# Kernel tuning notes

Hardware: AMD Instinct MI355X
Metric: run time of the kernel (lower is better)

Reference implementation:

```python
import jax, jax.numpy as jnp
import numpy as np

EPS = 1e-5
H = 128
NA = 300000
NB = 600000
NBRS = 6

def _bn(x, gamma, beta):
    # BatchNorm1d in training mode: batch stats over dim 0, biased variance
    mu = jnp.mean(x, axis=0)
    var = jnp.mean((x - mu) ** 2, axis=0)
    return gamma * (x - mu) * jax.lax.rsqrt(var + EPS) + beta

def _lin(x, w, b):
    return x @ w.T + b

def setup_inputs() -> dict:
    key = jax.random.key(0)
    ks = jax.random.split(key, 20)
    s = 1.0 / np.sqrt(H)
    d = {
        'atom_layer_input': jax.random.normal(ks[0], (NA, H), jnp.float32),
        'bond_layer_input': jax.random.normal(ks[1], (NB, H), jnp.float32),
        'atom_adjacency_graph': jax.random.randint(ks[2], (NA, NBRS), 0, NA, jnp.int32),
        'atom_bond_adjacency_graph': jax.random.randint(ks[3], (NA, NBRS), 0, NB, jnp.int32),
        'bond_atom_adjacency_graph': jax.random.randint(ks[4], (NB, 2), 0, NA, jnp.int32),
    }
    names = ['U', 'V', 'A', 'B', 'C']
    for i, n in enumerate(names):
        d[n + '_w'] = jax.random.uniform(ks[5 + 2 * i], (H, H), jnp.float32, -s, s)
        d[n + '_b'] = jax.random.uniform(ks[6 + 2 * i], (H,), jnp.float32, -s, s)
    d['bn_bond_gamma'] = jnp.ones((H,), jnp.float32)
    d['bn_bond_beta'] = jnp.zeros((H,), jnp.float32)
    d['bn_atom_gamma'] = jnp.ones((H,), jnp.float32)
    d['bn_atom_beta'] = jnp.zeros((H,), jnp.float32)
    return d

def reference(atom_layer_input, bond_layer_input, atom_adjacency_graph,
              atom_bond_adjacency_graph, bond_atom_adjacency_graph,
              U_w, U_b, V_w, V_b, A_w, A_b, B_w, B_b, C_w, C_b,
              bn_bond_gamma, bn_bond_beta, bn_atom_gamma, bn_atom_beta):
    # --- edge (bond) update ---
    ex = atom_layer_input[bond_atom_adjacency_graph[:, 0]]  # [NB, H]
    ey = atom_layer_input[bond_atom_adjacency_graph[:, 1]]  # [NB, H]
    edge_syn = _lin(bond_layer_input, A_w, A_b) + _lin(ex, B_w, B_b) + _lin(ey, C_w, C_b)
    edge_gates = jax.nn.sigmoid(edge_syn)                    # [NB, H]
    edge_syn_bn = _bn(edge_syn, bn_bond_gamma, bn_bond_beta)
    bond_layer_output = jax.nn.relu(edge_syn_bn)             # residual overwritten in source
    # --- node (atom) update ---
    nbr_feats = atom_layer_input[atom_adjacency_graph]       # [NA, 6, H] gather
    nbr_V = jnp.einsum('nkh,oh->nko', nbr_feats, V_w) + V_b  # [NA, 6, H]
    nbr_gates = edge_gates[atom_bond_adjacency_graph]        # [NA, 6, H] gather
    msg = jnp.sum(nbr_gates * nbr_V, axis=1)                 # [NA, H]
    atom_syn = _lin(atom_layer_input, U_w, U_b) + msg
    atom_syn_bn = _bn(atom_syn, bn_atom_gamma, bn_atom_beta)
    atom_layer_output = jax.nn.relu(atom_syn_bn) + atom_layer_input  # residual (atom_feature_dim==0)
    return (atom_layer_output, bond_layer_output)
```

## Files before the change

### kernel.cpp

```cpp
#include <hip/hip_runtime.h>
#include <hip/hip_bf16.h>


#define H   128
#define NA  300000
#define NB  600000
#define EPS 1e-5f

#define NTILE_A (NA / 32)
#define NTILE_B (NB / 32)
#define GRID_A  512
#define GRID_B  1024
#define EGRID   2048
#define LDSW    136

typedef __attribute__((ext_vector_type(4)))  float  f32x4;
typedef __attribute__((ext_vector_type(16))) float  f32x16;
typedef __attribute__((ext_vector_type(8)))  __bf16 bfv8;
typedef __attribute__((ext_vector_type(8)))  unsigned short u16x8;

static __device__ __forceinline__ unsigned short f2bf(float f) {
    unsigned u = __float_as_uint(f);
    u = (u + 0x7fffu + ((u >> 16) & 1u)) >> 16;
    return (unsigned short)u;
}
static __device__ __forceinline__ float bf2f(unsigned short s) {
    return __uint_as_float(((unsigned)s) << 16);
}

static __device__ __forceinline__ u16x8 pack2(f32x4 a, f32x4 b) {
    u16x8 w;
#pragma unroll
    for (int i = 0; i < 4; i++) { w[i] = f2bf(a[i]); w[i + 4] = f2bf(b[i]); }
    return w;
}

static __device__ __forceinline__ bfv8 load_frag(const float* __restrict__ p) {
    f32x4 a = *(const f32x4*)p, b = *(const f32x4*)(p + 4);
    bfv8 f;
#pragma unroll
    for (int i = 0; i < 4; i++) { f[i] = (__bf16)a[i]; f[i + 4] = (__bf16)b[i]; }
    return f;
}

__global__ __launch_bounds__(512, 4) void k_atom_gemm(
    const float* __restrict__ X,
    const float* __restrict__ Uw, const float* __restrict__ Vw,
    const float* __restrict__ Bw, const float* __restrict__ Cw,
    unsigned short* __restrict__ Uxo, unsigned short* __restrict__ Vxo,
    unsigned short* __restrict__ Bxo, unsigned short* __restrict__ Cxo)
{
    __shared__ unsigned short xs[2][32 * LDSW];
    __shared__ unsigned short es[2][32 * LDSW];

    const int tid   = threadIdx.x;
    const int lane  = tid & 63;
    const int w     = tid >> 6;
    const int ng    = w & 3;
    const int pair  = w >> 2;
    const int l31   = lane & 31;
    const int khalf = lane >> 5;

    const int wrow_off = (ng * 32 + l31) * H + khalf * 8;
    const int cperm    = ng * 32 + khalf * 16;

    const float* W0 = pair ? Bw : Uw;
    const float* W1 = pair ? Cw : Vw;

    bfv8 aw0[8], aw1[8];
#pragma unroll
    for (int k = 0; k < 8; k++) {
        aw0[k] = load_frag(W0 + wrow_off + k * 16);
        aw1[k] = load_frag(W1 + wrow_off + k * 16);
    }

    const int srow = tid >> 4, sseg = tid & 15;
    const int g = tid >> 8, ft = tid & 255;
    const int frow = ft >> 3, fseg = ft & 7;
    unsigned short* O0 = g ? Bxo : Uxo;
    unsigned short* O1 = g ? Cxo : Vxo;

    const int stride = gridDim.x;
    int t = blockIdx.x;

    f32x4 sl0, sl1;
    {
        const float* sp = X + (size_t)(t * 32 + srow) * H + sseg * 8;
        sl0 = *(const f32x4*)sp; sl1 = *(const f32x4*)(sp + 4);
    }
    *(u16x8*)&xs[0][srow * LDSW + sseg * 8] = pack2(sl0, sl1);
    __syncthreads();

    int p = 0;
#pragma unroll 1
    for (; t < NTILE_A; ) {
        const int tn = t + stride;
        const bool have = tn < NTILE_A;
        if (have) {
            const float* sp = X + (size_t)(tn * 32 + srow) * H + sseg * 8;
            sl0 = *(const f32x4*)sp; sl1 = *(const f32x4*)(sp + 4);
        }

        const unsigned short* xrow = &xs[p][l31 * LDSW + khalf * 8];
        unsigned short*       esw  = &es[pair][l31 * LDSW + cperm];
        const unsigned short* esr  = &es[g][frow * LDSW + fseg * 16];
        const size_t fbase = (size_t)(t * 32 + frow) * H + fseg * 16;

        {
            f32x16 acc;
#pragma unroll
            for (int i = 0; i < 16; i++) acc[i] = 0.0f;
#pragma unroll
            for (int k = 0; k < 8; k++) {
                bfv8 xf = *(const bfv8*)(xrow + k * 16);
                acc = __builtin_amdgcn_mfma_f32_32x32x16_bf16(aw0[k], xf, acc, 0, 0, 0);
            }
            u16x8 o0, o1;
#pragma unroll
            for (int v = 0; v < 8; v++) { o0[v] = f2bf(acc[v]); o1[v] = f2bf(acc[v + 8]); }
            *(u16x8*)esw       = o0;
            *(u16x8*)(esw + 8) = o1;
        }
        __syncthreads();

        f32x16 acc1;
#pragma unroll
        for (int i = 0; i < 16; i++) acc1[i] = 0.0f;
#pragma unroll
        for (int k = 0; k < 8; k++) {
            bfv8 xf = *(const bfv8*)(xrow + k * 16);
            acc1 = __builtin_amdgcn_mfma_f32_32x32x16_bf16(aw1[k], xf, acc1, 0, 0, 0);
        }
        {
            u16x8 e0 = *(const u16x8*)esr, e1 = *(const u16x8*)(esr + 8);
            *(u16x8*)(O0 + fbase)     = e0;
            *(u16x8*)(O0 + fbase + 8) = e1;
        }
        __syncthreads();

        {
            u16x8 o0, o1;
#pragma unroll
            for (int v = 0; v < 8; v++) { o0[v] = f2bf(acc1[v]); o1[v] = f2bf(acc1[v + 8]); }
            *(u16x8*)esw       = o0;
            *(u16x8*)(esw + 8) = o1;
        }
        __syncthreads();

        {
            u16x8 e0 = *(const u16x8*)esr, e1 = *(const u16x8*)(esr + 8);
            *(u16x8*)(O1 + fbase)     = e0;
            *(u16x8*)(O1 + fbase + 8) = e1;
        }
        if (have)
            *(u16x8*)&xs[p ^ 1][srow * LDSW + sseg * 8] = pack2(sl0, sl1);
        __syncthreads();
        p ^= 1;
        t = tn;
    }
}

__global__ __launch_bounds__(256, 4) void k_bond_gemm(
    const float* __restrict__ Xb,
    const float* __restrict__ Aw, const float* __restrict__ Ab,
    const float* __restrict__ Bb, const float* __restrict__ Cb,
    const int* __restrict__ g2,
    const unsigned short* __restrict__ Bx, const unsigned short* __restrict__ Cx,
    unsigned short* __restrict__ esyn,
    float* __restrict__ psum, float* __restrict__ psq)
{
    __shared__ unsigned short xs[2][32 * LDSW];
    __shared__ unsigned short es[32 * LDSW];
    __shared__ float bias_s[128];

    const int tid   = threadIdx.x;
    const int lane  = tid & 63;
    const int ng    = tid >> 6;
    const int l31   = lane & 31;
    const int khalf = lane >> 5;
    const int cperm = ng * 32 + khalf * 16;

    bfv8 aw[8];
    const float* wr = Aw + (ng * 32 + l31) * H + khalf * 8;
#pragma unroll
    for (int k = 0; k < 8; k++) aw[k] = load_frag(wr + k * 16);

    if (tid < 128) {
        const int pcol = tid;
        const int grp = pcol >> 5, r = pcol & 31, kh = r >> 4, wi = r & 15;
        const int ct = grp * 32 + (wi >> 2) * 8 + kh * 4 + (wi & 3);
        bias_s[pcol] = Ab[ct] + Bb[ct] + Cb[ct];
    }

    const int srow = tid >> 3, sseg = tid & 7;

    float fs[16], fq[16];
#pragma unroll
    for (int i = 0; i < 16; i++) { fs[i] = 0.f; fq[i] = 0.f; }

    const int stride = gridDim.x;
    int t = blockIdx.x;

    f32x4 sl[4];
    {
        const float* sp = Xb + (size_t)(t * 32 + srow) * H + sseg * 16;
#pragma unroll
        for (int i = 0; i < 4; i++) sl[i] = *(const f32x4*)(sp + 4 * i);
    }
    {
        unsigned short* d = &xs[0][srow * LDSW + sseg * 16];
        *(u16x8*)d       = pack2(sl[0], sl[1]);
        *(u16x8*)(d + 8) = pack2(sl[2], sl[3]);
    }
    int2 ggf = *(const int2*)(g2 + 2 * (size_t)(t * 32 + srow));
    __syncthreads();

    int p = 0;
#pragma unroll 1
    for (; t < NTILE_B; ) {
        const int tn = t + stride;
        const bool have = tn < NTILE_B;

        if (have) {
            const float* sp = Xb + (size_t)(tn * 32 + srow) * H + sseg * 16;
#pragma unroll
            for (int i = 0; i < 4; i++) sl[i] = *(const f32x4*)(sp + 4 * i);
        }

        {
            const unsigned short* xrow = &xs[p][l31 * LDSW + khalf * 8];
            f32x16 acc;
#pragma unroll
            for (int i = 0; i < 16; i++) acc[i] = 0.0f;
#pragma unroll
            for (int k = 0; k < 8; k++) {
                bfv8 xf = *(const bfv8*)(xrow + k * 16);
                acc = __builtin_amdgcn_mfma_f32_32x32x16_bf16(aw[k], xf, acc, 0, 0, 0);
            }
            u16x8 o0, o1;
#pragma unroll
            for (int v = 0; v < 8; v++) { o0[v] = f2bf(acc[v]); o1[v] = f2bf(acc[v + 8]); }
            unsigned short* esw = &es[l31 * LDSW + cperm];
            *(u16x8*)esw       = o0;
            *(u16x8*)(esw + 8) = o1;
        }

        const unsigned short* bxp = Bx + (size_t)ggf.x * H + sseg * 16;
        const unsigned short* cxp = Cx + (size_t)ggf.y * H + sseg * 16;
        u16x8 b0 = *(const u16x8*)bxp, b1 = *(const u16x8*)(bxp + 8);
        u16x8 c0 = *(const u16x8*)cxp, c1 = *(const u16x8*)(cxp + 8);
        if (have) ggf = *(const int2*)(g2 + 2 * (size_t)(tn * 32 + srow));
        __syncthreads();

        {
            const unsigned short* esr = &es[srow * LDSW + sseg * 16];
            u16x8 e0 = *(const u16x8*)esr, e1 = *(const u16x8*)(esr + 8);
            const float* bp = bias_s + sseg * 16;
            u16x8 w0, w1;
#pragma unroll
            for (int i = 0; i < 8; i++) {
                float v = bf2f(e0[i]) + bp[i] + bf2f(b0[i]) + bf2f(c0[i]);
                w0[i] = f2bf(v); fs[i] += v; fq[i] += v * v;
            }
#pragma unroll
            for (int i = 0; i < 8; i++) {
                float v = bf2f(e1[i]) + bp[8 + i] + bf2f(b1[i]) + bf2f(c1[i]);
                w1[i] = f2bf(v); fs[8 + i] += v; fq[8 + i] += v * v;
            }
            unsigned short* op = esyn + (size_t)(t * 32 + srow) * H + sseg * 16;
            *(u16x8*)op       = w0;
            *(u16x8*)(op + 8) = w1;
        }

        if (have) {
            unsigned short* d = &xs[p ^ 1][srow * LDSW + sseg * 16];
            *(u16x8*)d       = pack2(sl[0], sl[1]);
            *(u16x8*)(d + 8) = pack2(sl[2], sl[3]);
        }
        __syncthreads();
        p ^= 1;
        t = tn;
    }

    float* red = (float*)es;
    for (int i = 0; i < 16; i++) {
        __syncthreads();
        red[tid] = fs[i]; red[256 + tid] = fq[i];
        __syncthreads();
        if (tid < 8) {
            float S = 0.f, Q = 0.f;
            for (int r = 0; r < 32; r++) { S += red[r * 8 + tid]; Q += red[256 + r * 8 + tid]; }
            psum[(size_t)blockIdx.x * H + tid * 16 + i] = S;
            psq [(size_t)blockIdx.x * H + tid * 16 + i] = Q;
        }
    }
}

__global__ void k_bn_stats(const float* __restrict__ psum, const float* __restrict__ psq,
                           int nblk, float invN,
                           const float* __restrict__ gamma, const float* __restrict__ beta,
                           float* __restrict__ scale, float* __restrict__ shift)
{
    __shared__ float ls[256], lq[256];
    const int c = blockIdx.x;
    float s = 0.f, q = 0.f;
    for (int i = threadIdx.x; i < nblk; i += 256) {
        s += psum[(size_t)i * H + c];
        q += psq [(size_t)i * H + c];
    }
    ls[threadIdx.x] = s; lq[threadIdx.x] = q;
    __syncthreads();
    for (int off = 128; off > 0; off >>= 1) {
        if ((int)threadIdx.x < off) {
            ls[threadIdx.x] += ls[threadIdx.x + off];
            lq[threadIdx.x] += lq[threadIdx.x + off];
        }
        __syncthreads();
    }
    if (threadIdx.x == 0) {
        const int r = c & 31, kh = r >> 4, wi = r & 15;
        const int ct = (c & ~31) + (wi >> 2) * 8 + kh * 4 + (wi & 3);
        float mean = ls[0] * invN;
        float var  = lq[0] * invN - mean * mean;
        float sc   = gamma[ct] * rsqrtf(var + EPS);
        scale[c] = sc;
        shift[c] = beta[ct] - mean * sc;
    }
}

__global__ __launch_bounds__(256) void k_bond_out(const unsigned short* __restrict__ esyn,
                                                  float* __restrict__ y,
                                                  const float* __restrict__ scale,
                                                  const float* __restrict__ shift)
{
    const size_t total  = (size_t)NB * (H / 8);
    const size_t stride = (size_t)gridDim.x * 256;
    const int c0 = (threadIdx.x & 15) * 8;
    const f32x4 sc0 = *(const f32x4*)(scale + c0), sc1 = *(const f32x4*)(scale + c0 + 4);
    const f32x4 sh0 = *(const f32x4*)(shift + c0), sh1 = *(const f32x4*)(shift + c0 + 4);
    const int tc0 = (c0 & ~31) + (((c0 >> 2) & 3) * 8) + ((c0 >> 4) & 1) * 4;
    const int tc1 = tc0 + 8;
    for (size_t i = (size_t)blockIdx.x * 256 + threadIdx.x; i < total; i += stride) {
        u16x8 v = ((const u16x8*)esyn)[i];
        const size_t row = i >> 4;
        f32x4 o0, o1;
#pragma unroll
        for (int j = 0; j < 4; j++) {
            o0[j] = fmaxf(bf2f(v[j])     * sc0[j] + sh0[j], 0.0f);
            o1[j] = fmaxf(bf2f(v[j + 4]) * sc1[j] + sh1[j], 0.0f);
        }
        float* yp = y + row * H;
        *(f32x4*)(yp + tc0) = o0;
        *(f32x4*)(yp + tc1) = o1;
    }
}

__global__ __launch_bounds__(256) void k_atom_msg(
    const unsigned short* __restrict__ Ux,
    const unsigned short* __restrict__ Vx,
    const unsigned short* __restrict__ esyn,
    const int* __restrict__ adj,
    const int* __restrict__ abadj,
    const float* __restrict__ Ub, const float* __restrict__ Vb,
    unsigned short* __restrict__ syn_a,
    float* __restrict__ psum, float* __restrict__ psq)
{
    const int cg = threadIdx.x & 15;
    const int rh = threadIdx.x >> 4;
    const int c0 = cg * 8;
    const int tc0 = (c0 & ~31) + (((c0 >> 2) & 3) * 8) + ((c0 >> 4) & 1) * 4;
    const f32x4 ub0 = *(const f32x4*)(Ub + tc0), ub1 = *(const f32x4*)(Ub + tc0 + 8);
    const f32x4 vb0 = *(const f32x4*)(Vb + tc0), vb1 = *(const f32x4*)(Vb + tc0 + 8);

    float s[8], q[8];
#pragma unroll
    for (int j = 0; j < 8; j++) { s[j] = 0.f; q[j] = 0.f; }

    const int rstride = gridDim.x * 16;
    int r = blockIdx.x * 16 + rh;

    int2 A[3], Bv[3];
    if (r < NA) {
#pragma unroll
        for (int p = 0; p < 3; p++) {
            A[p]  = *(const int2*)(adj   + (size_t)r * 6 + 2 * p);
            Bv[p] = *(const int2*)(abadj + (size_t)r * 6 + 2 * p);
        }
    }

#pragma unroll 1
    for (; r < NA; ) {
        const int rn = r + rstride;

        const int ai[6] = {A[0].x, A[0].y, A[1].x, A[1].y, A[2].x, A[2].y};
        const int bi[6] = {Bv[0].x, Bv[0].y, Bv[1].x, Bv[1].y, Bv[2].x, Bv[2].y};

        u16x8 uv = *(const u16x8*)(Ux + (size_t)r * H + c0);

        if (rn < NA) {
#pragma unroll
            for (int p = 0; p < 3; p++) {
                A[p]  = *(const int2*)(adj   + (size_t)rn * 6 + 2 * p);
                Bv[p] = *(const int2*)(abadj + (size_t)rn * 6 + 2 * p);
            }
        }

        float v[8];
#pragma unroll
        for (int j = 0; j < 4; j++) {
            v[j]     = bf2f(uv[j])     + ub0[j];
            v[j + 4] = bf2f(uv[j + 4]) + ub1[j];
        }
#pragma unroll
        for (int k = 0; k < 6; k++) {
            u16x8 vx = *(const u16x8*)(Vx   + (size_t)ai[k] * H + c0);
            u16x8 es = *(const u16x8*)(esyn + (size_t)bi[k] * H + c0);
#pragma unroll
            for (int j = 0; j < 4; j++) {
                float g0 = 1.0f / (1.0f + __expf(-bf2f(es[j])));
                float g1 = 1.0f / (1.0f + __expf(-bf2f(es[j + 4])));
                v[j]     += g0 * (bf2f(vx[j])     + vb0[j]);
                v[j + 4] += g1 * (bf2f(vx[j + 4]) + vb1[j]);
            }
        }
        u16x8 ov;
#pragma unroll
        for (int j = 0; j < 8; j++) ov[j] = f2bf(v[j]);
        *(u16x8*)(syn_a + (size_t)r * H + c0) = ov;
#pragma unroll
        for (int j = 0; j < 8; j++) { s[j] += v[j]; q[j] += v[j] * v[j]; }

        r = rn;
    }

    __shared__ float ls[256][8], lq[256][8];
#pragma unroll
    for (int j = 0; j < 8; j++) { ls[threadIdx.x][j] = s[j]; lq[threadIdx.x][j] = q[j]; }
    __syncthreads();
    if (threadIdx.x < 128) {
        const int c = threadIdx.x, g = c >> 3, j = c & 7;
        float S = 0.f, Q = 0.f;
        for (int rg = 0; rg < 16; rg++) { S += ls[rg * 16 + g][j]; Q += lq[rg * 16 + g][j]; }
        psum[(size_t)blockIdx.x * H + c] = S;
        psq [(size_t)blockIdx.x * H + c] = Q;
    }
}

__global__ __launch_bounds__(256) void k_atom_out(const unsigned short* __restrict__ syn,
                                                  const float* __restrict__ xin,
                                                  float* __restrict__ y,
                                                  const float* __restrict__ scale,
                                                  const float* __restrict__ shift)
{
    const size_t total  = (size_t)NA * (H / 8);
    const size_t stride = (size_t)gridDim.x * 256;
    const int c0 = (threadIdx.x & 15) * 8;
    const f32x4 sc0 = *(const f32x4*)(scale + c0), sc1 = *(const f32x4*)(scale + c0 + 4);
    const f32x4 sh0 = *(const f32x4*)(shift + c0), sh1 = *(const f32x4*)(shift + c0 + 4);
    const int tc0 = (c0 & ~31) + (((c0 >> 2) & 3) * 8) + ((c0 >> 4) & 1) * 4;
    const int tc1 = tc0 + 8;
    for (size_t i = (size_t)blockIdx.x * 256 + threadIdx.x; i < total; i += stride) {
        u16x8 v = ((const u16x8*)syn)[i];
        const size_t row = i >> 4;
        const float* xp = xin + row * H;
        f32x4 x0 = *(const f32x4*)(xp + tc0), x1 = *(const f32x4*)(xp + tc1);
        f32x4 o0, o1;
#pragma unroll
        for (int j = 0; j < 4; j++) {
            o0[j] = fmaxf(bf2f(v[j])     * sc0[j] + sh0[j], 0.0f) + x0[j];
            o1[j] = fmaxf(bf2f(v[j + 4]) * sc1[j] + sh1[j], 0.0f) + x1[j];
        }
        float* yp = y + row * H;
        *(f32x4*)(yp + tc0) = o0;
        *(f32x4*)(yp + tc1) = o1;
    }
}

extern "C" void kernel_launch(void* const* d_in, const int* in_sizes, int n_in,
                              void* d_out, int out_size, void* d_ws, size_t ws_size,
                              hipStream_t stream)
{
    const float* X     = (const float*)d_in[0];
    const float* Xb    = (const float*)d_in[1];
    const int*   adj   = (const int*)d_in[2];
    const int*   abadj = (const int*)d_in[3];
    const int*   g2    = (const int*)d_in[4];
    const float* Uw = (const float*)d_in[5],  *Ub = (const float*)d_in[6];
    const float* Vw = (const float*)d_in[7],  *Vb = (const float*)d_in[8];
    const float* Aw = (const float*)d_in[9],  *Ab = (const float*)d_in[10];
    const float* Bw = (const float*)d_in[11], *Bb = (const float*)d_in[12];
    const float* Cw = (const float*)d_in[13], *Cb = (const float*)d_in[14];
    const float* gb = (const float*)d_in[15], *bb = (const float*)d_in[16];
    const float* ga = (const float*)d_in[17], *ba = (const float*)d_in[18];

    float* out_atom = (float*)d_out;
    float* out_bond = out_atom + (size_t)NA * H;

    char* ws = (char*)d_ws;
    size_t o = 0;
    unsigned short* Ux    = (unsigned short*)(ws + o); o += (size_t)NA * H * 2;
    unsigned short* Vx    = (unsigned short*)(ws + o); o += (size_t)NA * H * 2;
    unsigned short* Bx    = (unsigned short*)(ws + o); o += (size_t)NA * H * 2;
    unsigned short* Cx    = (unsigned short*)(ws + o); o += (size_t)NA * H * 2;
    unsigned short* esyn  = (unsigned short*)(ws + o); o += (size_t)NB * H * 2;
    unsigned short* syn_a = (unsigned short*)(ws + o); o += (size_t)NA * H * 2;
    float* psum_b = (float*)(ws + o);  o += (size_t)EGRID * H * 4;
    float* psq_b  = (float*)(ws + o);  o += (size_t)EGRID * H * 4;
    float* psum_a = (float*)(ws + o);  o += (size_t)EGRID * H * 4;
    float* psq_a  = (float*)(ws + o);  o += (size_t)EGRID * H * 4;
    float* scale_b = (float*)(ws + o); o += 512;
    float* shift_b = (float*)(ws + o); o += 512;
    float* scale_a = (float*)(ws + o); o += 512;
    float* shift_a = (float*)(ws + o); o += 512;
    (void)o; (void)ws_size; (void)in_sizes; (void)n_in; (void)out_size;

    k_atom_gemm<<<GRID_A, 512, 0, stream>>>(X, Uw, Vw, Bw, Cw, Ux, Vx, Bx, Cx);
    k_bond_gemm<<<GRID_B, 256, 0, stream>>>(Xb, Aw, Ab, Bb, Cb, g2, Bx, Cx, esyn,
                                            psum_b, psq_b);
    k_bn_stats<<<H, 256, 0, stream>>>(psum_b, psq_b, GRID_B, 1.0f / NB, gb, bb, scale_b, shift_b);
    k_bond_out<<<EGRID, 256, 0, stream>>>(esyn, out_bond, scale_b, shift_b);
    k_atom_msg<<<EGRID, 256, 0, stream>>>(Ux, Vx, esyn, adj, abadj, Ub, Vb, syn_a, psum_a, psq_a);
    k_bn_stats<<<H, 256, 0, stream>>>(psum_a, psq_a, EGRID, 1.0f / NA, ga, ba, scale_a, shift_a);
    k_atom_out<<<EGRID, 256, 0, stream>>>(syn_a, X, out_atom, scale_a, shift_a);
}
```

Before: 604.3 us.

## Fuse bond output and atom message kernels into one grid; add nontemporal streaming

```diff
diff --git a/kernel.cpp b/kernel.cpp
--- a/kernel.cpp
+++ b/kernel.cpp
@@ -9,9 +9,12 @@
 
 #define NTILE_A (NA / 32)
 #define NTILE_B (NB / 32)
-#define GRID_A  512
-#define GRID_B  1024
+#define GRID_A  1024
+#define GRID_B  1536
 #define EGRID   2048
+#define BOUT_BLKS 768
+#define MSG_BLKS  1280
+#define FUSED_GRID (BOUT_BLKS + MSG_BLKS)
 #define LDSW    136
 
 typedef __attribute__((ext_vector_type(4)))  float  f32x4;
@@ -26,6 +29,13 @@
 }
 static __device__ __forceinline__ float bf2f(unsigned short s) {
     return __uint_as_float(((unsigned)s) << 16);
+}
+
+static __device__ __forceinline__ f32x4 nt_load4(const float* p) {
+    return __builtin_nontemporal_load((const f32x4*)p);
+}
+static __device__ __forceinline__ void nt_store4(float* p, f32x4 v) {
+    __builtin_nontemporal_store(v, (f32x4*)p);
 }
 
 static __device__ __forceinline__ u16x8 pack2(f32x4 a, f32x4 b) {
@@ -86,7 +96,7 @@
     f32x4 sl0, sl1;
     {
         const float* sp = X + (size_t)(t * 32 + srow) * H + sseg * 8;
-        sl0 = *(const f32x4*)sp; sl1 = *(const f32x4*)(sp + 4);
+        sl0 = nt_load4(sp); sl1 = nt_load4(sp + 4);
     }
     *(u16x8*)&xs[0][srow * LDSW + sseg * 8] = pack2(sl0, sl1);
     __syncthreads();
@@ -98,7 +108,7 @@
         const bool have = tn < NTILE_A;
         if (have) {
             const float* sp = X + (size_t)(tn * 32 + srow) * H + sseg * 8;
-            sl0 = *(const f32x4*)sp; sl1 = *(const f32x4*)(sp + 4);
+            sl0 = nt_load4(sp); sl1 = nt_load4(sp + 4);
         }
 
         const unsigned short* xrow = &xs[p][l31 * LDSW + khalf * 8];
@@ -205,7 +215,7 @@
     {
         const float* sp = Xb + (size_t)(t * 32 + srow) * H + sseg * 16;
 #pragma unroll
-        for (int i = 0; i < 4; i++) sl[i] = *(const f32x4*)(sp + 4 * i);
+        for (int i = 0; i < 4; i++) sl[i] = nt_load4(sp + 4 * i);
     }
     {
         unsigned short* d = &xs[0][srow * LDSW + sseg * 16];
@@ -224,7 +234,7 @@
         if (have) {
             const float* sp = Xb + (size_t)(tn * 32 + srow) * H + sseg * 16;
 #pragma unroll
-            for (int i = 0; i < 4; i++) sl[i] = *(const f32x4*)(sp + 4 * i);
+            for (int i = 0; i < 4; i++) sl[i] = nt_load4(sp + 4 * i);
         }
 
         {
@@ -328,43 +338,45 @@
     }
 }
 
-__global__ __launch_bounds__(256) void k_bond_out(const unsigned short* __restrict__ esyn,
-                                                  float* __restrict__ y,
-                                                  const float* __restrict__ scale,
-                                                  const float* __restrict__ shift)
-{
-    const size_t total  = (size_t)NB * (H / 8);
-    const size_t stride = (size_t)gridDim.x * 256;
-    const int c0 = (threadIdx.x & 15) * 8;
-    const f32x4 sc0 = *(const f32x4*)(scale + c0), sc1 = *(const f32x4*)(scale + c0 + 4);
-    const f32x4 sh0 = *(const f32x4*)(shift + c0), sh1 = *(const f32x4*)(shift + c0 + 4);
-    const int tc0 = (c0 & ~31) + (((c0 >> 2) & 3) * 8) + ((c0 >> 4) & 1) * 4;
-    const int tc1 = tc0 + 8;
-    for (size_t i = (size_t)blockIdx.x * 256 + threadIdx.x; i < total; i += stride) {
-        u16x8 v = ((const u16x8*)esyn)[i];
-        const size_t row = i >> 4;
-        f32x4 o0, o1;
-#pragma unroll
-        for (int j = 0; j < 4; j++) {
-            o0[j] = fmaxf(bf2f(v[j])     * sc0[j] + sh0[j], 0.0f);
-            o1[j] = fmaxf(bf2f(v[j + 4]) * sc1[j] + sh1[j], 0.0f);
-        }
-        float* yp = y + row * H;
-        *(f32x4*)(yp + tc0) = o0;
-        *(f32x4*)(yp + tc1) = o1;
-    }
-}
-
-__global__ __launch_bounds__(256) void k_atom_msg(
+__global__ __launch_bounds__(256) void k_bout_amsg(
+    const unsigned short* __restrict__ esyn,
+    float* __restrict__ out_bond,
+    const float* __restrict__ scale, const float* __restrict__ shift,
     const unsigned short* __restrict__ Ux,
     const unsigned short* __restrict__ Vx,
-    const unsigned short* __restrict__ esyn,
     const int* __restrict__ adj,
     const int* __restrict__ abadj,
     const float* __restrict__ Ub, const float* __restrict__ Vb,
     unsigned short* __restrict__ syn_a,
     float* __restrict__ psum, float* __restrict__ psq)
 {
+    __shared__ float ls[256][8], lq[256][8];
+
+    if (blockIdx.x < BOUT_BLKS) {
+        const size_t total  = (size_t)NB * (H / 8);
+        const size_t stride = (size_t)BOUT_BLKS * 256;
+        const int c0 = (threadIdx.x & 15) * 8;
+        const f32x4 sc0 = *(const f32x4*)(scale + c0), sc1 = *(const f32x4*)(scale + c0 + 4);
+        const f32x4 sh0 = *(const f32x4*)(shift + c0), sh1 = *(const f32x4*)(shift + c0 + 4);
+        const int tc0 = (c0 & ~31) + (((c0 >> 2) & 3) * 8) + ((c0 >> 4) & 1) * 4;
+        const int tc1 = tc0 + 8;
+        for (size_t i = (size_t)blockIdx.x * 256 + threadIdx.x; i < total; i += stride) {
+            u16x8 v = ((const u16x8*)esyn)[i];
+            const size_t row = i >> 4;
+            f32x4 o0, o1;
+#pragma unroll
+            for (int j = 0; j < 4; j++) {
+                o0[j] = fmaxf(bf2f(v[j])     * sc0[j] + sh0[j], 0.0f);
+                o1[j] = fmaxf(bf2f(v[j + 4]) * sc1[j] + sh1[j], 0.0f);
+            }
+            float* yp = out_bond + row * H;
+            nt_store4(yp + tc0, o0);
+            nt_store4(yp + tc1, o1);
+        }
+        return;
+    }
+
+    const int bid = blockIdx.x - BOUT_BLKS;
     const int cg = threadIdx.x & 15;
     const int rh = threadIdx.x >> 4;
     const int c0 = cg * 8;
@@ -376,8 +388,8 @@
 #pragma unroll
     for (int j = 0; j < 8; j++) { s[j] = 0.f; q[j] = 0.f; }
 
-    const int rstride = gridDim.x * 16;
-    int r = blockIdx.x * 16 + rh;
+    const int rstride = MSG_BLKS * 16;
+    int r = bid * 16 + rh;
 
     int2 A[3], Bv[3];
     if (r < NA) {
@@ -433,7 +445,6 @@
         r = rn;
     }
 
-    __shared__ float ls[256][8], lq[256][8];
 #pragma unroll
     for (int j = 0; j < 8; j++) { ls[threadIdx.x][j] = s[j]; lq[threadIdx.x][j] = q[j]; }
     __syncthreads();
@@ -441,8 +452,8 @@
         const int c = threadIdx.x, g = c >> 3, j = c & 7;
         float S = 0.f, Q = 0.f;
         for (int rg = 0; rg < 16; rg++) { S += ls[rg * 16 + g][j]; Q += lq[rg * 16 + g][j]; }
-        psum[(size_t)blockIdx.x * H + c] = S;
-        psq [(size_t)blockIdx.x * H + c] = Q;
+        psum[(size_t)bid * H + c] = S;
+        psq [(size_t)bid * H + c] = Q;
     }
 }
 
@@ -463,7 +474,7 @@
         u16x8 v = ((const u16x8*)syn)[i];
         const size_t row = i >> 4;
         const float* xp = xin + row * H;
-        f32x4 x0 = *(const f32x4*)(xp + tc0), x1 = *(const f32x4*)(xp + tc1);
+        f32x4 x0 = nt_load4(xp + tc0), x1 = nt_load4(xp + tc1);
         f32x4 o0, o1;
 #pragma unroll
         for (int j = 0; j < 4; j++) {
@@ -471,8 +482,8 @@
             o1[j] = fmaxf(bf2f(v[j + 4]) * sc1[j] + sh1[j], 0.0f) + x1[j];
         }
         float* yp = y + row * H;
-        *(f32x4*)(yp + tc0) = o0;
-        *(f32x4*)(yp + tc1) = o1;
+        nt_store4(yp + tc0, o0);
+        nt_store4(yp + tc1, o1);
     }
 }
 
@@ -518,8 +529,9 @@
     k_bond_gemm<<<GRID_B, 256, 0, stream>>>(Xb, Aw, Ab, Bb, Cb, g2, Bx, Cx, esyn,
                                             psum_b, psq_b);
     k_bn_stats<<<H, 256, 0, stream>>>(psum_b, psq_b, GRID_B, 1.0f / NB, gb, bb, scale_b, shift_b);
-    k_bond_out<<<EGRID, 256, 0, stream>>>(esyn, out_bond, scale_b, shift_b);
-    k_atom_msg<<<EGRID, 256, 0, stream>>>(Ux, Vx, esyn, adj, abadj, Ub, Vb, syn_a, psum_a, psq_a);
-    k_bn_stats<<<H, 256, 0, stream>>>(psum_a, psq_a, EGRID, 1.0f / NA, ga, ba, scale_a, shift_a);
+    k_bout_amsg<<<FUSED_GRID, 256, 0, stream>>>(esyn, out_bond, scale_b, shift_b,
+                                                Ux, Vx, adj, abadj, Ub, Vb,
+                                                syn_a, psum_a, psq_a);
+    k_bn_stats<<<H, 256, 0, stream>>>(psum_a, psq_a, MSG_BLKS, 1.0f / NA, ga, ba, scale_a, shift_a);
     k_atom_out<<<EGRID, 256, 0, stream>>>(syn_a, X, out_atom, scale_a, shift_a);
 }
```

After: 669.9 us. 1.11x slower.

## Compute bond B/C projections in bond GEMM from gathered atom rows instead of precomputing

Applied to the files above, without the earlier changes.

```diff
diff --git a/kernel.cpp b/kernel.cpp
--- a/kernel.cpp
+++ b/kernel.cpp
@@ -46,9 +46,7 @@
 __global__ __launch_bounds__(512, 4) void k_atom_gemm(
     const float* __restrict__ X,
     const float* __restrict__ Uw, const float* __restrict__ Vw,
-    const float* __restrict__ Bw, const float* __restrict__ Cw,
-    unsigned short* __restrict__ Uxo, unsigned short* __restrict__ Vxo,
-    unsigned short* __restrict__ Bxo, unsigned short* __restrict__ Cxo)
+    unsigned short* __restrict__ Uxo, unsigned short* __restrict__ Vxo)
 {
     __shared__ unsigned short xs[2][32 * LDSW];
     __shared__ unsigned short es[2][32 * LDSW];
@@ -64,21 +62,15 @@
     const int wrow_off = (ng * 32 + l31) * H + khalf * 8;
     const int cperm    = ng * 32 + khalf * 16;
 
-    const float* W0 = pair ? Bw : Uw;
-    const float* W1 = pair ? Cw : Vw;
-
-    bfv8 aw0[8], aw1[8];
-#pragma unroll
-    for (int k = 0; k < 8; k++) {
-        aw0[k] = load_frag(W0 + wrow_off + k * 16);
-        aw1[k] = load_frag(W1 + wrow_off + k * 16);
-    }
+    const float* W = pair ? Vw : Uw;
+    bfv8 aw[8];
+#pragma unroll
+    for (int k = 0; k < 8; k++) aw[k] = load_frag(W + wrow_off + k * 16);
 
     const int srow = tid >> 4, sseg = tid & 15;
     const int g = tid >> 8, ft = tid & 255;
     const int frow = ft >> 3, fseg = ft & 7;
-    unsigned short* O0 = g ? Bxo : Uxo;
-    unsigned short* O1 = g ? Cxo : Vxo;
+    unsigned short* O = g ? Vxo : Uxo;
 
     const int stride = gridDim.x;
     int t = blockIdx.x;
@@ -101,56 +93,31 @@
             sl0 = *(const f32x4*)sp; sl1 = *(const f32x4*)(sp + 4);
         }
 
-        const unsigned short* xrow = &xs[p][l31 * LDSW + khalf * 8];
-        unsigned short*       esw  = &es[pair][l31 * LDSW + cperm];
-        const unsigned short* esr  = &es[g][frow * LDSW + fseg * 16];
-        const size_t fbase = (size_t)(t * 32 + frow) * H + fseg * 16;
-
         {
+            const unsigned short* xrow = &xs[p][l31 * LDSW + khalf * 8];
             f32x16 acc;
 #pragma unroll
             for (int i = 0; i < 16; i++) acc[i] = 0.0f;
 #pragma unroll
             for (int k = 0; k < 8; k++) {
                 bfv8 xf = *(const bfv8*)(xrow + k * 16);
-                acc = __builtin_amdgcn_mfma_f32_32x32x16_bf16(aw0[k], xf, acc, 0, 0, 0);
+                acc = __builtin_amdgcn_mfma_f32_32x32x16_bf16(aw[k], xf, acc, 0, 0, 0);
             }
             u16x8 o0, o1;
 #pragma unroll
             for (int v = 0; v < 8; v++) { o0[v] = f2bf(acc[v]); o1[v] = f2bf(acc[v + 8]); }
+            unsigned short* esw = &es[pair][l31 * LDSW + cperm];
             *(u16x8*)esw       = o0;
             *(u16x8*)(esw + 8) = o1;
         }
         __syncthreads();
 
-        f32x16 acc1;
-#pragma unroll
-        for (int i = 0; i < 16; i++) acc1[i] = 0.0f;
-#pragma unroll
-        for (int k = 0; k < 8; k++) {
-            bfv8 xf = *(const bfv8*)(xrow + k * 16);
-            acc1 = __builtin_amdgcn_mfma_f32_32x32x16_bf16(aw1[k], xf, acc1, 0, 0, 0);
-        }
         {
+            const unsigned short* esr = &es[g][frow * LDSW + fseg * 16];
             u16x8 e0 = *(const u16x8*)esr, e1 = *(const u16x8*)(esr + 8);
-            *(u16x8*)(O0 + fbase)     = e0;
-            *(u16x8*)(O0 + fbase + 8) = e1;
-        }
-        __syncthreads();
-
-        {
-            u16x8 o0, o1;
-#pragma unroll
-            for (int v = 0; v < 8; v++) { o0[v] = f2bf(acc1[v]); o1[v] = f2bf(acc1[v + 8]); }
-            *(u16x8*)esw       = o0;
-            *(u16x8*)(esw + 8) = o1;
-        }
-        __syncthreads();
-
-        {
-            u16x8 e0 = *(const u16x8*)esr, e1 = *(const u16x8*)(esr + 8);
-            *(u16x8*)(O1 + fbase)     = e0;
-            *(u16x8*)(O1 + fbase + 8) = e1;
+            const size_t fbase = (size_t)(t * 32 + frow) * H + fseg * 16;
+            *(u16x8*)(O + fbase)     = e0;
+            *(u16x8*)(O + fbase + 8) = e1;
         }
         if (have)
             *(u16x8*)&xs[p ^ 1][srow * LDSW + sseg * 8] = pack2(sl0, sl1);
@@ -160,16 +127,17 @@
     }
 }
 
-__global__ __launch_bounds__(256, 4) void k_bond_gemm(
-    const float* __restrict__ Xb,
-    const float* __restrict__ Aw, const float* __restrict__ Ab,
-    const float* __restrict__ Bb, const float* __restrict__ Cb,
+__global__ __launch_bounds__(256, 2) void k_bond_gemm(
+    const float* __restrict__ Xb, const float* __restrict__ X,
+    const float* __restrict__ Aw, const float* __restrict__ Bw,
+    const float* __restrict__ Cw,
+    const float* __restrict__ Ab, const float* __restrict__ Bb,
+    const float* __restrict__ Cb,
     const int* __restrict__ g2,
-    const unsigned short* __restrict__ Bx, const unsigned short* __restrict__ Cx,
     unsigned short* __restrict__ esyn,
     float* __restrict__ psum, float* __restrict__ psq)
 {
-    __shared__ unsigned short xs[2][32 * LDSW];
+    __shared__ unsigned short ts[3][32 * LDSW];
     __shared__ unsigned short es[32 * LDSW];
     __shared__ float bias_s[128];
 
@@ -180,10 +148,14 @@
     const int khalf = lane >> 5;
     const int cperm = ng * 32 + khalf * 16;
 
-    bfv8 aw[8];
-    const float* wr = Aw + (ng * 32 + l31) * H + khalf * 8;
-#pragma unroll
-    for (int k = 0; k < 8; k++) aw[k] = load_frag(wr + k * 16);
+    const int wro = (ng * 32 + l31) * H + khalf * 8;
+    bfv8 awA[8], awB[8], awC[8];
+#pragma unroll
+    for (int k = 0; k < 8; k++) {
+        awA[k] = load_frag(Aw + wro + k * 16);
+        awB[k] = load_frag(Bw + wro + k * 16);
+        awC[k] = load_frag(Cw + wro + k * 16);
+    }
 
     if (tid < 128) {
         const int pcol = tid;
@@ -201,42 +173,67 @@
     const int stride = gridDim.x;
     int t = blockIdx.x;
 
-    f32x4 sl[4];
+    u16x8 rx0, rx1, re0, re1, ry0, ry1;
+    int2 gg;
+
     {
+        int2 g0 = *(const int2*)(g2 + 2 * (size_t)(t * 32 + srow));
         const float* sp = Xb + (size_t)(t * 32 + srow) * H + sseg * 16;
-#pragma unroll
-        for (int i = 0; i < 4; i++) sl[i] = *(const f32x4*)(sp + 4 * i);
-    }
-    {
-        unsigned short* d = &xs[0][srow * LDSW + sseg * 16];
-        *(u16x8*)d       = pack2(sl[0], sl[1]);
-        *(u16x8*)(d + 8) = pack2(sl[2], sl[3]);
-    }
-    int2 ggf = *(const int2*)(g2 + 2 * (size_t)(t * 32 + srow));
-    __syncthreads();
-
-    int p = 0;
+        rx0 = pack2(*(const f32x4*)sp,          *(const f32x4*)(sp + 4));
+        rx1 = pack2(*(const f32x4*)(sp + 8),    *(const f32x4*)(sp + 12));
+        const float* ep = X + (size_t)g0.x * H + sseg * 16;
+        re0 = pack2(*(const f32x4*)ep,          *(const f32x4*)(ep + 4));
+        re1 = pack2(*(const f32x4*)(ep + 8),    *(const f32x4*)(ep + 12));
+        const float* yp = X + (size_t)g0.y * H + sseg * 16;
+        ry0 = pack2(*(const f32x4*)yp,          *(const f32x4*)(yp + 4));
+        ry1 = pack2(*(const f32x4*)(yp + 8),    *(const f32x4*)(yp + 12));
+        const int tnx = t + stride;
+        if (tnx < NTILE_B) gg = *(const int2*)(g2 + 2 * (size_t)(tnx * 32 + srow));
+    }
+
 #pragma unroll 1
     for (; t < NTILE_B; ) {
         const int tn = t + stride;
         const bool have = tn < NTILE_B;
 
+        {
+            const int off = srow * LDSW + sseg * 16;
+            *(u16x8*)&ts[0][off]     = rx0; *(u16x8*)&ts[0][off + 8] = rx1;
+            *(u16x8*)&ts[1][off]     = re0; *(u16x8*)&ts[1][off + 8] = re1;
+            *(u16x8*)&ts[2][off]     = ry0; *(u16x8*)&ts[2][off + 8] = ry1;
+        }
+        __syncthreads();
+
         if (have) {
             const float* sp = Xb + (size_t)(tn * 32 + srow) * H + sseg * 16;
-#pragma unroll
-            for (int i = 0; i < 4; i++) sl[i] = *(const f32x4*)(sp + 4 * i);
+            rx0 = pack2(*(const f32x4*)sp,       *(const f32x4*)(sp + 4));
+            rx1 = pack2(*(const f32x4*)(sp + 8), *(const f32x4*)(sp + 12));
+            const float* ep = X + (size_t)gg.x * H + sseg * 16;
+            re0 = pack2(*(const f32x4*)ep,       *(const f32x4*)(ep + 4));
+            re1 = pack2(*(const f32x4*)(ep + 8), *(const f32x4*)(ep + 12));
+            const float* yp = X + (size_t)gg.y * H + sseg * 16;
+            ry0 = pack2(*(const f32x4*)yp,       *(const f32x4*)(yp + 4));
+            ry1 = pack2(*(const f32x4*)(yp + 8), *(const f32x4*)(yp + 12));
+            const int tnn = tn + stride;
+            if (tnn < NTILE_B) gg = *(const int2*)(g2 + 2 * (size_t)(tnn * 32 + srow));
         }
 
         {
-            const unsigned short* xrow = &xs[p][l31 * LDSW + khalf * 8];
+            const unsigned short* x0 = &ts[0][l31 * LDSW + khalf * 8];
+            const unsigned short* x1 = &ts[1][l31 * LDSW + khalf * 8];
+            const unsigned short* x2 = &ts[2][l31 * LDSW + khalf * 8];
             f32x16 acc;
 #pragma unroll
             for (int i = 0; i < 16; i++) acc[i] = 0.0f;
 #pragma unroll
-            for (int k = 0; k < 8; k++) {
-                bfv8 xf = *(const bfv8*)(xrow + k * 16);
-                acc = __builtin_amdgcn_mfma_f32_32x32x16_bf16(aw[k], xf, acc, 0, 0, 0);
-            }
+            for (int k = 0; k < 8; k++)
+                acc = __builtin_amdgcn_mfma_f32_32x32x16_bf16(awA[k], *(const bfv8*)(x0 + k * 16), acc, 0, 0, 0);
+#pragma unroll
+            for (int k = 0; k < 8; k++)
+                acc = __builtin_amdgcn_mfma_f32_32x32x16_bf16(awB[k], *(const bfv8*)(x1 + k * 16), acc, 0, 0, 0);
+#pragma unroll
+            for (int k = 0; k < 8; k++)
+                acc = __builtin_amdgcn_mfma_f32_32x32x16_bf16(awC[k], *(const bfv8*)(x2 + k * 16), acc, 0, 0, 0);
             u16x8 o0, o1;
 #pragma unroll
             for (int v = 0; v < 8; v++) { o0[v] = f2bf(acc[v]); o1[v] = f2bf(acc[v + 8]); }
@@ -244,12 +241,6 @@
             *(u16x8*)esw       = o0;
             *(u16x8*)(esw + 8) = o1;
         }
-
-        const unsigned short* bxp = Bx + (size_t)ggf.x * H + sseg * 16;
-        const unsigned short* cxp = Cx + (size_t)ggf.y * H + sseg * 16;
-        u16x8 b0 = *(const u16x8*)bxp, b1 = *(const u16x8*)(bxp + 8);
-        u16x8 c0 = *(const u16x8*)cxp, c1 = *(const u16x8*)(cxp + 8);
-        if (have) ggf = *(const int2*)(g2 + 2 * (size_t)(tn * 32 + srow));
         __syncthreads();
 
         {
@@ -259,26 +250,18 @@
             u16x8 w0, w1;
 #pragma unroll
             for (int i = 0; i < 8; i++) {
-                float v = bf2f(e0[i]) + bp[i] + bf2f(b0[i]) + bf2f(c0[i]);
+                float v = bf2f(e0[i]) + bp[i];
                 w0[i] = f2bf(v); fs[i] += v; fq[i] += v * v;
             }
 #pragma unroll
             for (int i = 0; i < 8; i++) {
-                float v = bf2f(e1[i]) + bp[8 + i] + bf2f(b1[i]) + bf2f(c1[i]);
+                float v = bf2f(e1[i]) + bp[8 + i];
                 w1[i] = f2bf(v); fs[8 + i] += v; fq[8 + i] += v * v;
             }
             unsigned short* op = esyn + (size_t)(t * 32 + srow) * H + sseg * 16;
             *(u16x8*)op       = w0;
             *(u16x8*)(op + 8) = w1;
         }
-
-        if (have) {
-            unsigned short* d = &xs[p ^ 1][srow * LDSW + sseg * 16];
-            *(u16x8*)d       = pack2(sl[0], sl[1]);
-            *(u16x8*)(d + 8) = pack2(sl[2], sl[3]);
-        }
-        __syncthreads();
-        p ^= 1;
         t = tn;
     }
 
@@ -500,8 +483,6 @@
     size_t o = 0;
     unsigned short* Ux    = (unsigned short*)(ws + o); o += (size_t)NA * H * 2;
     unsigned short* Vx    = (unsigned short*)(ws + o); o += (size_t)NA * H * 2;
-    unsigned short* Bx    = (unsigned short*)(ws + o); o += (size_t)NA * H * 2;
-    unsigned short* Cx    = (unsigned short*)(ws + o); o += (size_t)NA * H * 2;
     unsigned short* esyn  = (unsigned short*)(ws + o); o += (size_t)NB * H * 2;
     unsigned short* syn_a = (unsigned short*)(ws + o); o += (size_t)NA * H * 2;
     float* psum_b = (float*)(ws + o);  o += (size_t)EGRID * H * 4;
@@ -514,9 +495,9 @@
     float* shift_a = (float*)(ws + o); o += 512;
     (void)o; (void)ws_size; (void)in_sizes; (void)n_in; (void)out_size;
 
-    k_atom_gemm<<<GRID_A, 512, 0, stream>>>(X, Uw, Vw, Bw, Cw, Ux, Vx, Bx, Cx);
-    k_bond_gemm<<<GRID_B, 256, 0, stream>>>(Xb, Aw, Ab, Bb, Cb, g2, Bx, Cx, esyn,
-                                            psum_b, psq_b);
+    k_atom_gemm<<<GRID_A, 512, 0, stream>>>(X, Uw, Vw, Ux, Vx);
+    k_bond_gemm<<<GRID_B, 256, 0, stream>>>(Xb, X, Aw, Bw, Cw, Ab, Bb, Cb, g2,
+                                            esyn, psum_b, psq_b);
     k_bn_stats<<<H, 256, 0, stream>>>(psum_b, psq_b, GRID_B, 1.0f / NB, gb, bb, scale_b, shift_b);
     k_bond_out<<<EGRID, 256, 0, stream>>>(esyn, out_bond, scale_b, shift_b);
     k_atom_msg<<<EGRID, 256, 0, stream>>>(Ux, Vx, esyn, adj, abadj, Ub, Vb, syn_a, psum_a, psq_a);
```

After: 602.7 us. No clear change (-0.3%).
